# Performance work log

Hardware: AMD Instinct MI355X
Metric: run time of the kernel (lower is better)

Reference implementation:

```python
import jax, jax.numpy as jnp
import numpy as np

H, KVH, D, HID = 32, 32, 128, 4096
THETA = 10000.0
EPS = 1e-5


def setup_inputs() -> dict:
    key = jax.random.key(0)
    ks = jax.random.split(key, 7)
    T = 2048
    return {
        "positions": jnp.arange(T, dtype=jnp.int32),
        "hidden_states": jax.random.normal(ks[0], (T, HID), dtype=jnp.float32),
        "w_qkv": jax.random.normal(ks[1], ((H + 2 * KVH) * D, HID), dtype=jnp.float32) * 0.02,
        "w_o": jax.random.normal(ks[2], (HID, H * D), dtype=jnp.float32) * 0.02,
        "q_norm_w": jax.random.uniform(ks[3], (H, D), dtype=jnp.float32),
        "q_norm_b": jax.random.normal(ks[4], (H, D), dtype=jnp.float32) * 0.02,
        "k_norm_w": jax.random.uniform(ks[5], (KVH, D), dtype=jnp.float32),
        "k_norm_b": jax.random.normal(ks[6], (KVH, D), dtype=jnp.float32) * 0.02,
    }


def _per_head_ln(x, w, b):
    # x: [T, H, D]; layer_norm over last dim without affine, then *w + b (per head)
    mu = jnp.mean(x, axis=-1, keepdims=True)
    var = jnp.mean(jnp.square(x - mu), axis=-1, keepdims=True)
    xn = (x - mu) * jax.lax.rsqrt(var + EPS)
    return xn * w + b


def _rope(x, positions):
    # neox-style rotate-half RoPE; x: [T, H, D]
    half = D // 2
    inv_freq = 1.0 / (THETA ** (jnp.arange(0, D, 2, dtype=jnp.float32) / D))  # [D/2]
    freqs = positions.astype(jnp.float32)[:, None] * inv_freq  # [T, D/2]
    cos = jnp.cos(freqs)[:, None, :]  # [T, 1, D/2]
    sin = jnp.sin(freqs)[:, None, :]
    x1, x2 = x[..., :half], x[..., half:]
    return jnp.concatenate([x1 * cos - x2 * sin, x2 * cos + x1 * sin], axis=-1)


def reference(positions, hidden_states, w_qkv, w_o, q_norm_w, q_norm_b, k_norm_w, k_norm_b):
    T = hidden_states.shape[0]
    qkv = hidden_states @ w_qkv.T  # [T, (H+2*KVH)*D]
    q, k, v = jnp.split(qkv, [H * D, (H + KVH) * D], axis=-1)
    q = q.reshape(T, H, D)
    k = k.reshape(T, KVH, D)
    v = v.reshape(T, KVH, D)
    q = _per_head_ln(q, q_norm_w, q_norm_b)
    k = _per_head_ln(k, k_norm_w, k_norm_b)
    q = _rope(q, positions)
    k = _rope(k, positions)
    scale = D ** -0.5
    scores = jnp.einsum("qhd,khd->hqk", q, k) * scale  # [H, T, T]
    causal = jnp.tril(jnp.ones((T, T), dtype=bool))
    scores = jnp.where(causal, scores, jnp.finfo(scores.dtype).min)
    probs = jax.nn.softmax(scores, axis=-1)
    attn = jnp.einsum("hqk,khd->qhd", probs, v).reshape(T, H * D)
    return attn @ w_o.T  # [T, HID]
```

## Files before the change

kernel.cpp:

```cpp
#include <hip/hip_runtime.h>
#include <cstdint>

typedef unsigned short u16;
typedef __attribute__((ext_vector_type(8))) __bf16 bf16x8;
typedef __attribute__((ext_vector_type(4))) float f32x4;

__device__ __forceinline__ u16 f2bf(float f) {
  unsigned int u = __builtin_bit_cast(unsigned int, f);
  unsigned int r = (u + 0x7fffu + ((u >> 16) & 1u)) >> 16;
  return (u16)r;
}
__device__ __forceinline__ float bf2f(u16 u) {
  return __builtin_bit_cast(float, (unsigned int)u << 16);
}

__device__ __forceinline__ void gload16(const u16* g, u16* l) {
  __builtin_amdgcn_global_load_lds((const __attribute__((address_space(1))) void*)g,
                                   (__attribute__((address_space(3))) void*)l, 16, 0, 0);
}

__device__ __forceinline__ int swz64i(int row, int col) {
  return row * 64 + (((col & 0x38) ^ ((row & 7) << 3)) | (col & 7));
}
__device__ __forceinline__ int swz128i(int row, int col) {
  return row * 128 + (((col & 0x78) ^ ((row & 7) << 3)) | (col & 7));
}

__global__ __launch_bounds__(256) void cvt_bf16_kernel(const float* __restrict__ in,
                                                       u16* __restrict__ out, long n4) {
  long i = (long)blockIdx.x * 256 + threadIdx.x;
  long stride = (long)gridDim.x * 256;
  const float4* in4 = (const float4*)in;
  uint2* out2 = (uint2*)out;
  for (long k = i; k < n4; k += stride) {
    float4 v = in4[k];
    uint2 o;
    o.x = (unsigned int)f2bf(v.x) | ((unsigned int)f2bf(v.y) << 16);
    o.y = (unsigned int)f2bf(v.z) | ((unsigned int)f2bf(v.w) << 16);
    out2[k] = o;
  }
}

__global__ __launch_bounds__(512, 2) void gemm192(const u16* __restrict__ A,
                                                  const u16* __restrict__ B,
                                                  u16* __restrict__ C,
                                                  int Ndim, int Kdim) {
  extern __shared__ __align__(16) u16 lds[];
  const int tid = threadIdx.x;
  const int lane = tid & 63, wave = tid >> 6;
  const int wr = wave >> 2, wc = wave & 3;
  const int l15 = lane & 15, l4 = lane >> 4;
  const int gx = gridDim.x;
  int lin = blockIdx.y * gx + blockIdx.x;
  const int xcd = lin & 7, ii = lin >> 3;
  const int bx = xcd * (gx >> 3) + (ii >> 3), by = ii & 7;
  const long arow = (long)by * 256, brow = (long)bx * 192;
  const int NT = Kdim >> 6;

  const int rowt = tid >> 3;
  const int koff = ((tid & 7) ^ (rowt & 7)) * 8;
  const u16* gA[4];
  const u16* gB[3];
  #pragma unroll
  for (int r = 0; r < 4; ++r) gA[r] = A + (size_t)(arow + rowt + r * 64) * Kdim + koff;
  #pragma unroll
  for (int r = 0; r < 3; ++r) gB[r] = B + (size_t)(brow + rowt + r * 64) * Kdim + koff;
  u16* const ldsB = lds + 32768;

  auto STA = [&](int u) {
    u16* d = lds + (u & 1) * 16384 + tid * 8;
    #pragma unroll
    for (int r = 0; r < 4; ++r) gload16(gA[r] + (size_t)u * 64, d + r * 4096);
  };
  auto STB = [&](int u) {
    u16* d = ldsB + (u & 1) * 12288 + tid * 8;
    #pragma unroll
    for (int r = 0; r < 3; ++r) gload16(gB[r] + (size_t)u * 64, d + r * 4096);
  };

  bf16x8 af[8][2], bfr[2];
  f32x4 acc[8][3] = {};
  int cks[2];
  #pragma unroll
  for (int kc = 0; kc < 2; ++kc) cks[kc] = (((kc * 4 + l4) ^ (l15 & 7)) * 8);

  auto LDA = [&](int u) {
    const u16* base = lds + (u & 1) * 16384 + (wr * 128 + l15) * 64;
    #pragma unroll
    for (int m = 0; m < 8; ++m)
      #pragma unroll
      for (int kc = 0; kc < 2; ++kc)
        af[m][kc] = *(const bf16x8*)(base + m * 1024 + cks[kc]);
  };
  auto LDB = [&](int u, int nh) {
    const u16* base = ldsB + (u & 1) * 12288 + (wc * 48 + nh * 16 + l15) * 64;
    #pragma unroll
    for (int kc = 0; kc < 2; ++kc)
      bfr[kc] = *(const bf16x8*)(base + cks[kc]);
  };
  auto MMQ = [&](int nh) {
    #pragma unroll
    for (int kc = 0; kc < 2; ++kc)
      #pragma unroll
      for (int m = 0; m < 8; ++m)
        acc[m][nh] = __builtin_amdgcn_mfma_f32_16x16x32_bf16(af[m][kc], bfr[kc],
                                                             acc[m][nh], 0, 0, 0);
  };

#define PH_BEGIN() do { __builtin_amdgcn_s_barrier();                         \
    asm volatile("s_waitcnt lgkmcnt(0)" ::: "memory");                        \
    __builtin_amdgcn_sched_barrier(0);                                        \
    __builtin_amdgcn_s_setprio(1); } while (0)
#define PH_END() do { __builtin_amdgcn_s_setprio(0);                          \
    __builtin_amdgcn_s_barrier(); } while (0)

  STA(0); STB(0); STA(1);
  asm volatile("s_waitcnt vmcnt(4)" ::: "memory");
  __builtin_amdgcn_s_barrier();

  for (int u = 0; u < NT; ++u) {
    LDA(u); LDB(u, 0);
    if (u + 1 < NT) STB(u + 1);
    PH_BEGIN(); MMQ(0); PH_END();
    LDB(u, 1);
    if (u + 2 < NT) STA(u + 2);
    PH_BEGIN(); MMQ(1); PH_END();
    LDB(u, 2);
    PH_BEGIN(); MMQ(2);
    __builtin_amdgcn_s_setprio(0);
    if (u + 2 < NT) { asm volatile("s_waitcnt vmcnt(4)" ::: "memory"); }
    else            { asm volatile("s_waitcnt vmcnt(0)" ::: "memory"); }
    __builtin_amdgcn_s_barrier();
  }
#undef PH_BEGIN
#undef PH_END

  #pragma unroll
  for (int m = 0; m < 8; ++m)
    #pragma unroll
    for (int nh = 0; nh < 3; ++nh)
      #pragma unroll
      for (int j = 0; j < 4; ++j) {
        long r = arow + wr * 128 + m * 16 + l4 * 4 + j;
        long c = brow + wc * 48 + nh * 16 + l15;
        C[r * Ndim + c] = f2bf(acc[m][nh][j]);
      }
}

__global__ __launch_bounds__(512, 2) void gemm256(const u16* __restrict__ A,
                                                  const u16* __restrict__ B,
                                                  float* __restrict__ C,
                                                  int Ndim, int Kdim) {
  extern __shared__ __align__(16) u16 lds[];
  const int tid = threadIdx.x;
  const int lane = tid & 63, wave = tid >> 6;
  const int wr = wave >> 2, wc = wave & 3;
  const int l15 = lane & 15, l4 = lane >> 4;
  const int gx = gridDim.x;
  int lin = blockIdx.y * gx + blockIdx.x;
  const int xcd = lin & 7, ii = lin >> 3;
  const int bx = xcd * (gx >> 3) + (ii >> 3), by = ii & 7;
  const long arow = (long)by * 256, brow = (long)bx * 128;
  const int NT = Kdim >> 6;

  const int rowt = tid >> 3;
  const int koff = ((tid & 7) ^ (rowt & 7)) * 8;
  const u16* gA[4];
  const u16* gB[2];
  #pragma unroll
  for (int r = 0; r < 4; ++r) gA[r] = A + (size_t)(arow + rowt + r * 64) * Kdim + koff;
  #pragma unroll
  for (int r = 0; r < 2; ++r) gB[r] = B + (size_t)(brow + rowt + r * 64) * Kdim + koff;

  auto STA = [&](int u) {
    u16* d = lds + (u % 3) * 16384 + tid * 8;
    #pragma unroll
    for (int r = 0; r < 4; ++r) gload16(gA[r] + (size_t)u * 64, d + r * 4096);
  };
  auto STB = [&](int u) {
    u16* d = lds + 49152 + (u & 1) * 8192 + tid * 8;
    #pragma unroll
    for (int r = 0; r < 2; ++r) gload16(gB[r] + (size_t)u * 64, d + r * 4096);
  };

  bf16x8 af[4][2], bfr[2][2];
  f32x4 acc[8][2] = {};
  int cks[2];
  #pragma unroll
  for (int kc = 0; kc < 2; ++kc) cks[kc] = (((kc * 4 + l4) ^ (l15 & 7)) * 8);

  auto LDA = [&](int u, int mh) {
    const u16* base = lds + (u % 3) * 16384 + (wr * 128 + mh * 64 + l15) * 64;
    #pragma unroll
    for (int m = 0; m < 4; ++m)
      #pragma unroll
      for (int kc = 0; kc < 2; ++kc)
        af[m][kc] = *(const bf16x8*)(base + m * 1024 + cks[kc]);
  };
  auto LDB = [&](int u) {
    const u16* base = lds + 49152 + (u & 1) * 8192 + (wc * 32 + l15) * 64;
    #pragma unroll
    for (int n = 0; n < 2; ++n)
      #pragma unroll
      for (int kc = 0; kc < 2; ++kc)
        bfr[n][kc] = *(const bf16x8*)(base + n * 1024 + cks[kc]);
  };
  auto MM = [&](int mh) {
    #pragma unroll
    for (int kc = 0; kc < 2; ++kc)
      #pragma unroll
      for (int m = 0; m < 4; ++m)
        #pragma unroll
        for (int n = 0; n < 2; ++n)
          acc[mh * 4 + m][n] =
            __builtin_amdgcn_mfma_f32_16x16x32_bf16(af[m][kc], bfr[n][kc],
                                                    acc[mh * 4 + m][n], 0, 0, 0);
  };

#define PH_BEGIN() do { __builtin_amdgcn_s_barrier();                         \
    asm volatile("s_waitcnt lgkmcnt(0)" ::: "memory");                        \
    __builtin_amdgcn_sched_barrier(0);                                        \
    __builtin_amdgcn_s_setprio(1); } while (0)

  STA(0); STB(0); STA(1); STB(1);
  asm volatile("s_waitcnt vmcnt(6)" ::: "memory");
  __builtin_amdgcn_s_barrier();

  for (int u = 0; u < NT; ++u) {
    LDA(u, 0); LDB(u);
    if (u + 2 < NT) STA(u + 2);
    PH_BEGIN(); MM(0);
    __builtin_amdgcn_s_setprio(0);
    __builtin_amdgcn_s_barrier();
    LDA(u, 1);
    if (u + 2 < NT) STB(u + 2);
    PH_BEGIN(); MM(1);
    __builtin_amdgcn_s_setprio(0);
    if (u + 2 < NT) { asm volatile("s_waitcnt vmcnt(6)" ::: "memory"); }
    else if (u + 1 < NT) { asm volatile("s_waitcnt vmcnt(0)" ::: "memory"); }
    __builtin_amdgcn_s_barrier();
  }
#undef PH_BEGIN

  #pragma unroll
  for (int M = 0; M < 8; ++M)
    #pragma unroll
    for (int n = 0; n < 2; ++n)
      #pragma unroll
      for (int j = 0; j < 4; ++j) {
        long r = arow + wr * 128 + M * 16 + l4 * 4 + j;
        long c = brow + wc * 32 + n * 16 + l15;
        C[r * Ndim + c] = acc[M][n][j];
      }
}

__global__ __launch_bounds__(256) void ln_rope_kernel(
    const u16* __restrict__ qkv, const int* __restrict__ pos,
    const float* __restrict__ qw, const float* __restrict__ qb2,
    const float* __restrict__ kw, const float* __restrict__ kb2,
    u16* __restrict__ qo, u16* __restrict__ ko, u16* __restrict__ vo, int T) {
  const int hh = blockIdx.x;
  const int t = blockIdx.y * 4 + (threadIdx.x >> 6);
  const int lane = threadIdx.x & 63;
  const u16* src = qkv + (size_t)t * 12288 + hh * 128;
  u16 u1 = src[lane], u2 = src[lane + 64];
  if (hh >= 64) {
    u16* dst = vo + ((size_t)(hh - 64) * T + t) * 128;
    dst[lane] = u1; dst[lane + 64] = u2;
    return;
  }
  float x1 = bf2f(u1), x2 = bf2f(u2);
  float s = x1 + x2;
  #pragma unroll
  for (int off = 32; off; off >>= 1) s += __shfl_xor(s, off);
  float mu = s * (1.0f / 128.0f);
  float d1 = x1 - mu, d2 = x2 - mu;
  float vs = d1 * d1 + d2 * d2;
  #pragma unroll
  for (int off = 32; off; off >>= 1) vs += __shfl_xor(vs, off);
  float rstd = rsqrtf(vs * (1.0f / 128.0f) + 1e-5f);
  bool isq = hh < 32;
  int hl = isq ? hh : hh - 32;
  const float* w = (isq ? qw : kw) + hl * 128;
  const float* b = (isq ? qb2 : kb2) + hl * 128;
  float y1 = d1 * rstd * w[lane] + b[lane];
  float y2 = d2 * rstd * w[lane + 64] + b[lane + 64];
  float p = (float)pos[t];
  float invf = exp2f((float)lane * (-13.287712379549449f / 64.0f));
  float fr = p * invf;
  float sn, cs;
  __sincosf(fr, &sn, &cs);
  float o1 = y1 * cs - y2 * sn;
  float o2 = y2 * cs + y1 * sn;
  if (isq) {
    const float sc = 0.08838834764831845f;
    o1 *= sc; o2 *= sc;
    u16* dst = qo + ((size_t)hl * T + t) * 128;
    dst[lane] = f2bf(o1); dst[lane + 64] = f2bf(o2);
  } else {
    u16* dst = ko + ((size_t)hl * T + t) * 128;
    dst[lane] = f2bf(o1); dst[lane + 64] = f2bf(o2);
  }
}

__global__ __launch_bounds__(256, 2) void flash_kernel(
    const u16* __restrict__ qb, const u16* __restrict__ kb,
    const u16* __restrict__ vb, u16* __restrict__ attn, int T) {
  __shared__ __align__(16) u16 Ks[64 * 128];
  __shared__ __align__(16) u16 Vt[128 * 64];
  __shared__ __align__(16) u16 Ps[4][32 * 64];
  const int tid = threadIdx.x;
  const int lane = tid & 63, wave = tid >> 6;
  const int l15 = lane & 15, l4 = lane >> 4;
  const int h = blockIdx.y;
  const int qbase = blockIdx.x * 128;
  const u16* Q  = qb + (size_t)h * T * 128;
  const u16* Kp = kb + (size_t)h * T * 128;
  const u16* Vp = vb + (size_t)h * T * 128;
  const int rK0 = tid >> 4, d8k = (tid & 15) * 8;

  bf16x8 qf[2][4];
  #pragma unroll
  for (int mi = 0; mi < 2; ++mi)
    #pragma unroll
    for (int kc = 0; kc < 4; ++kc)
      qf[mi][kc] = *(const bf16x8*)&Q[(size_t)(qbase + mi * 64 + wave * 16 + l15) * 128 + kc * 32 + l4 * 8];

  float m_st[2][4], l_st[2][4];
  f32x4 o[2][8] = {};
  #pragma unroll
  for (int mi = 0; mi < 2; ++mi)
    #pragma unroll
    for (int j = 0; j < 4; ++j) { m_st[mi][j] = -1e30f; l_st[mi][j] = 0.0f; }

  const int ntile = (qbase + 128) / 64;
  uint4 kr[4], vr[4];
  #pragma unroll
  for (int c = 0; c < 4; ++c) {
    kr[c] = *(const uint4*)&Kp[(size_t)(rK0 + 16 * c) * 128 + d8k];
    vr[c] = *(const uint4*)&Vp[(size_t)lane * 128 + (wave + 4 * c) * 8];
  }
  for (int kt = 0; kt < ntile; ++kt) {
    const int kbase = kt * 64;
    #pragma unroll
    for (int c = 0; c < 4; ++c) {
      *(uint4*)&Ks[swz128i(rK0 + 16 * c, d8k)] = kr[c];
      const u16* pv = (const u16*)&vr[c];
      int dv = (wave + 4 * c) * 8;
      #pragma unroll
      for (int j = 0; j < 8; ++j) Vt[swz64i(dv + j, lane)] = pv[j];
    }
    __syncthreads();
    if (kt + 1 < ntile) {
      const int nb = kbase + 64;
      #pragma unroll
      for (int c = 0; c < 4; ++c) {
        kr[c] = *(const uint4*)&Kp[(size_t)(nb + rK0 + 16 * c) * 128 + d8k];
        vr[c] = *(const uint4*)&Vp[(size_t)(nb + lane) * 128 + (wave + 4 * c) * 8];
      }
    }
    #pragma unroll
    for (int mi = 0; mi < 2; ++mi) {
      const int r0 = qbase + mi * 64 + wave * 16;
      if (kbase <= r0 + 15) {
        f32x4 s[4] = {};
        __builtin_amdgcn_s_setprio(1);
        #pragma unroll
        for (int kc = 0; kc < 4; ++kc)
          #pragma unroll
          for (int nj = 0; nj < 4; ++nj) {
            bf16x8 kf = *(const bf16x8*)&Ks[swz128i(nj * 16 + l15, kc * 32 + l4 * 8)];
            s[nj] = __builtin_amdgcn_mfma_f32_16x16x32_bf16(qf[mi][kc], kf, s[nj], 0, 0, 0);
          }
        __builtin_amdgcn_s_setprio(0);
        if (kbase + 63 > r0) {
          #pragma unroll
          for (int nj = 0; nj < 4; ++nj)
            #pragma unroll
            for (int j = 0; j < 4; ++j) {
              int r = r0 + l4 * 4 + j;
              int cc = kbase + nj * 16 + l15;
              if (cc > r) s[nj][j] = -1e30f;
            }
        }
        float vmax[4];
        float dmax = -1e30f;
        #pragma unroll
        for (int j = 0; j < 4; ++j) {
          float v = fmaxf(fmaxf(s[0][j], s[1][j]), fmaxf(s[2][j], s[3][j]));
          #pragma unroll
          for (int off = 1; off < 16; off <<= 1) v = fmaxf(v, __shfl_xor(v, off));
          vmax[j] = v;
          dmax = fmaxf(dmax, v - m_st[mi][j]);
        }
        if (!__all(dmax <= 8.0f)) {
          #pragma unroll
          for (int j = 0; j < 4; ++j) {
            float mn = fmaxf(m_st[mi][j], vmax[j]);
            float scl = __expf(m_st[mi][j] - mn);
            m_st[mi][j] = mn;
            l_st[mi][j] *= scl;
            #pragma unroll
            for (int nf = 0; nf < 8; ++nf) o[mi][nf][j] *= scl;
          }
        }
        float sum[4] = {0.f, 0.f, 0.f, 0.f};
        #pragma unroll
        for (int nj = 0; nj < 4; ++nj)
          #pragma unroll
          for (int j = 0; j < 4; ++j) {
            float p = __expf(s[nj][j] - m_st[mi][j]);
            s[nj][j] = p;
            sum[j] += p;
          }
        #pragma unroll
        for (int j = 0; j < 4; ++j) {
          #pragma unroll
          for (int off = 1; off < 16; off <<= 1) sum[j] += __shfl_xor(sum[j], off);
          l_st[mi][j] += sum[j];
        }
        #pragma unroll
        for (int nj = 0; nj < 4; ++nj)
          #pragma unroll
          for (int j = 0; j < 4; ++j)
            Ps[wave][swz64i(mi * 16 + l4 * 4 + j, nj * 16 + l15)] = f2bf(s[nj][j]);
        asm volatile("s_waitcnt lgkmcnt(0)" ::: "memory");
        __builtin_amdgcn_sched_barrier(0);
        __builtin_amdgcn_s_setprio(1);
        #pragma unroll
        for (int kc = 0; kc < 2; ++kc) {
          bf16x8 pf = *(const bf16x8*)&Ps[wave][swz64i(mi * 16 + l15, kc * 32 + l4 * 8)];
          #pragma unroll
          for (int nf = 0; nf < 8; ++nf) {
            bf16x8 vf = *(const bf16x8*)&Vt[swz64i(nf * 16 + l15, kc * 32 + l4 * 8)];
            o[mi][nf] = __builtin_amdgcn_mfma_f32_16x16x32_bf16(pf, vf, o[mi][nf], 0, 0, 0);
          }
        }
        __builtin_amdgcn_s_setprio(0);
      }
    }
    __syncthreads();
  }
  #pragma unroll
  for (int mi = 0; mi < 2; ++mi) {
    float rl[4];
    #pragma unroll
    for (int j = 0; j < 4; ++j) rl[j] = 1.0f / l_st[mi][j];
    #pragma unroll
    for (int nf = 0; nf < 8; ++nf)
      #pragma unroll
      for (int j = 0; j < 4; ++j) {
        int r = qbase + mi * 64 + wave * 16 + l4 * 4 + j;
        int cc = h * 128 + nf * 16 + l15;
        attn[(size_t)r * 4096 + cc] = f2bf(o[mi][nf][j] * rl[j]);
      }
  }
}

extern "C" void kernel_launch(void* const* d_in, const int* in_sizes, int n_in,
                              void* d_out, int out_size, void* d_ws, size_t ws_size,
                              hipStream_t stream) {
  const int* positions = (const int*)d_in[0];
  const float* hidden  = (const float*)d_in[1];
  const float* w_qkv   = (const float*)d_in[2];
  const float* w_o     = (const float*)d_in[3];
  const float* qnw     = (const float*)d_in[4];
  const float* qnb     = (const float*)d_in[5];
  const float* knw     = (const float*)d_in[6];
  const float* knb     = (const float*)d_in[7];
  float* out = (float*)d_out;

  const int T = in_sizes[0];
  const int HID = 4096, NQKV = 12288, H = 32;

  char* ws = (char*)d_ws;
  u16* hid_bf  = (u16*)ws;
  u16* wreg    = (u16*)(ws + (size_t)T * HID * 2);
  u16* qkv_bf  = (u16*)(ws + (size_t)T * HID * 2 + (size_t)NQKV * HID * 2);

  u16* q_bf  = wreg;
  u16* k_bf  = q_bf + (size_t)H * T * 128;
  u16* v_bf  = k_bf + (size_t)H * T * 128;
  u16* at_bf = v_bf + (size_t)H * T * 128;
  u16* wo_bf = at_bf + (size_t)T * 4096;

  hipFuncSetAttribute(reinterpret_cast<const void*>(&gemm192),
                      hipFuncAttributeMaxDynamicSharedMemorySize, 114688);
  hipFuncSetAttribute(reinterpret_cast<const void*>(&gemm256),
                      hipFuncAttributeMaxDynamicSharedMemorySize, 131072);

  cvt_bf16_kernel<<<2048, 256, 0, stream>>>(hidden, hid_bf, (long)T * HID / 4);
  cvt_bf16_kernel<<<4096, 256, 0, stream>>>(w_qkv, wreg, (long)NQKV * HID / 4);
  gemm192<<<dim3(NQKV / 192, T / 256), 512, 114688, stream>>>(hid_bf, wreg, qkv_bf, NQKV, HID);
  ln_rope_kernel<<<dim3(96, T / 4), 256, 0, stream>>>(qkv_bf, positions, qnw, qnb, knw, knb,
                                                      q_bf, k_bf, v_bf, T);
  cvt_bf16_kernel<<<2048, 256, 0, stream>>>(w_o, wo_bf, (long)HID * HID / 4);
  flash_kernel<<<dim3(T / 128, H), 256, 0, stream>>>(q_bf, k_bf, v_bf, at_bf, T);
  gemm256<<<dim3(HID / 128, T / 256), 512, 131072, stream>>>(at_bf, wo_bf, out, HID, HID);
}
```

Measured before the change: 543.9 us.

## Triple-buffer gemm192 A tiles and pair causal q-tiles in 512-thread flash blocks

gemm192 now triple-buffers its A tile and splits each K step into two phases over 64-row halves of A instead of three phases over B column groups, so one B fragment load serves both phases. The flash kernel now runs 512 threads per block, with waves 0-3 handling a late causal q-tile and waves 4-7 an early one while sharing K/V tiles in LDS. This balances causal work across blocks and halves the K/V loads per query. The cost is more LDS per block, which may lower occupancy, and the early-tile waves sit idle on tiles beyond their causal limit.

```diff
diff --git a/kernel.cpp b/kernel.cpp
--- a/kernel.cpp
+++ b/kernel.cpp
@@ -65,10 +65,10 @@
   for (int r = 0; r < 4; ++r) gA[r] = A + (size_t)(arow + rowt + r * 64) * Kdim + koff;
   #pragma unroll
   for (int r = 0; r < 3; ++r) gB[r] = B + (size_t)(brow + rowt + r * 64) * Kdim + koff;
-  u16* const ldsB = lds + 32768;
+  u16* const ldsB = lds + 49152;
 
   auto STA = [&](int u) {
-    u16* d = lds + (u & 1) * 16384 + tid * 8;
+    u16* d = lds + (u % 3) * 16384 + tid * 8;
     #pragma unroll
     for (int r = 0; r < 4; ++r) gload16(gA[r] + (size_t)u * 64, d + r * 4096);
   };
@@ -78,33 +78,37 @@
     for (int r = 0; r < 3; ++r) gload16(gB[r] + (size_t)u * 64, d + r * 4096);
   };
 
-  bf16x8 af[8][2], bfr[2];
+  bf16x8 af[4][2], bfr[3][2];
   f32x4 acc[8][3] = {};
   int cks[2];
   #pragma unroll
   for (int kc = 0; kc < 2; ++kc) cks[kc] = (((kc * 4 + l4) ^ (l15 & 7)) * 8);
 
-  auto LDA = [&](int u) {
-    const u16* base = lds + (u & 1) * 16384 + (wr * 128 + l15) * 64;
-    #pragma unroll
-    for (int m = 0; m < 8; ++m)
+  auto LDA4 = [&](int u, int mh) {
+    const u16* base = lds + (u % 3) * 16384 + (wr * 128 + mh * 64 + l15) * 64;
+    #pragma unroll
+    for (int m = 0; m < 4; ++m)
       #pragma unroll
       for (int kc = 0; kc < 2; ++kc)
         af[m][kc] = *(const bf16x8*)(base + m * 1024 + cks[kc]);
   };
-  auto LDB = [&](int u, int nh) {
-    const u16* base = ldsB + (u & 1) * 12288 + (wc * 48 + nh * 16 + l15) * 64;
+  auto LDBall = [&](int u) {
+    const u16* base = ldsB + (u & 1) * 12288 + (wc * 48 + l15) * 64;
+    #pragma unroll
+    for (int nh = 0; nh < 3; ++nh)
+      #pragma unroll
+      for (int kc = 0; kc < 2; ++kc)
+        bfr[nh][kc] = *(const bf16x8*)(base + nh * 1024 + cks[kc]);
+  };
+  auto MM24 = [&](int mh) {
     #pragma unroll
     for (int kc = 0; kc < 2; ++kc)
-      bfr[kc] = *(const bf16x8*)(base + cks[kc]);
-  };
-  auto MMQ = [&](int nh) {
-    #pragma unroll
-    for (int kc = 0; kc < 2; ++kc)
-      #pragma unroll
-      for (int m = 0; m < 8; ++m)
-        acc[m][nh] = __builtin_amdgcn_mfma_f32_16x16x32_bf16(af[m][kc], bfr[kc],
-                                                             acc[m][nh], 0, 0, 0);
+      #pragma unroll
+      for (int m = 0; m < 4; ++m)
+        #pragma unroll
+        for (int nh = 0; nh < 3; ++nh)
+          acc[mh * 4 + m][nh] = __builtin_amdgcn_mfma_f32_16x16x32_bf16(
+              af[m][kc], bfr[nh][kc], acc[mh * 4 + m][nh], 0, 0, 0);
   };
 
 #define PH_BEGIN() do { __builtin_amdgcn_s_barrier();                         \
@@ -119,14 +123,12 @@
   __builtin_amdgcn_s_barrier();
 
   for (int u = 0; u < NT; ++u) {
-    LDA(u); LDB(u, 0);
+    LDA4(u, 0); LDBall(u);
     if (u + 1 < NT) STB(u + 1);
-    PH_BEGIN(); MMQ(0); PH_END();
-    LDB(u, 1);
+    PH_BEGIN(); MM24(0); PH_END();
+    LDA4(u, 1);
     if (u + 2 < NT) STA(u + 2);
-    PH_BEGIN(); MMQ(1); PH_END();
-    LDB(u, 2);
-    PH_BEGIN(); MMQ(2);
+    PH_BEGIN(); MM24(1);
     __builtin_amdgcn_s_setprio(0);
     if (u + 2 < NT) { asm volatile("s_waitcnt vmcnt(4)" ::: "memory"); }
     else            { asm volatile("s_waitcnt vmcnt(0)" ::: "memory"); }
@@ -303,28 +305,34 @@
   }
 }
 
-__global__ __launch_bounds__(256, 2) void flash_kernel(
+__global__ __launch_bounds__(512, 2) void flash_kernel(
     const u16* __restrict__ qb, const u16* __restrict__ kb,
     const u16* __restrict__ vb, u16* __restrict__ attn, int T) {
-  __shared__ __align__(16) u16 Ks[64 * 128];
-  __shared__ __align__(16) u16 Vt[128 * 64];
-  __shared__ __align__(16) u16 Ps[4][32 * 64];
+  extern __shared__ __align__(16) u16 flds[];
+  u16* const Ks = flds;
+  u16* const Vt = flds + 8192;
+  u16* const Ps = flds + 16384;
   const int tid = threadIdx.x;
   const int lane = tid & 63, wave = tid >> 6;
+  const int wl = wave & 3;
   const int l15 = lane & 15, l4 = lane >> 4;
   const int h = blockIdx.y;
-  const int qbase = blockIdx.x * 128;
+  const int nqt = T >> 7;
+  const int qt = (wave < 4) ? (nqt - 1 - blockIdx.x) : blockIdx.x;
+  const int qbase = qt * 128;
   const u16* Q  = qb + (size_t)h * T * 128;
   const u16* Kp = kb + (size_t)h * T * 128;
   const u16* Vp = vb + (size_t)h * T * 128;
-  const int rK0 = tid >> 4, d8k = (tid & 15) * 8;
+  const int rK = tid >> 4, d8k = (tid & 15) * 8;
+  const int rv = tid & 63, dv0 = (tid >> 6) * 8;
+  u16* const Pw = Ps + wave * 2048;
 
   bf16x8 qf[2][4];
   #pragma unroll
   for (int mi = 0; mi < 2; ++mi)
     #pragma unroll
     for (int kc = 0; kc < 4; ++kc)
-      qf[mi][kc] = *(const bf16x8*)&Q[(size_t)(qbase + mi * 64 + wave * 16 + l15) * 128 + kc * 32 + l4 * 8];
+      qf[mi][kc] = *(const bf16x8*)&Q[(size_t)(qbase + mi * 64 + wl * 16 + l15) * 128 + kc * 32 + l4 * 8];
 
   float m_st[2][4], l_st[2][4];
   f32x4 o[2][8] = {};
@@ -333,35 +341,34 @@
     #pragma unroll
     for (int j = 0; j < 4; ++j) { m_st[mi][j] = -1e30f; l_st[mi][j] = 0.0f; }
 
-  const int ntile = (qbase + 128) / 64;
-  uint4 kr[4], vr[4];
-  #pragma unroll
-  for (int c = 0; c < 4; ++c) {
-    kr[c] = *(const uint4*)&Kp[(size_t)(rK0 + 16 * c) * 128 + d8k];
-    vr[c] = *(const uint4*)&Vp[(size_t)lane * 128 + (wave + 4 * c) * 8];
+  const int ntile = 2 * (nqt - 1 - blockIdx.x) + 2;
+  uint4 kr[2], vr[2];
+  #pragma unroll
+  for (int c = 0; c < 2; ++c) {
+    kr[c] = *(const uint4*)&Kp[(size_t)(rK + 32 * c) * 128 + d8k];
+    vr[c] = *(const uint4*)&Vp[(size_t)rv * 128 + dv0 + 64 * c];
   }
   for (int kt = 0; kt < ntile; ++kt) {
     const int kbase = kt * 64;
     #pragma unroll
-    for (int c = 0; c < 4; ++c) {
-      *(uint4*)&Ks[swz128i(rK0 + 16 * c, d8k)] = kr[c];
+    for (int c = 0; c < 2; ++c) {
+      *(uint4*)&Ks[swz128i(rK + 32 * c, d8k)] = kr[c];
       const u16* pv = (const u16*)&vr[c];
-      int dv = (wave + 4 * c) * 8;
-      #pragma unroll
-      for (int j = 0; j < 8; ++j) Vt[swz64i(dv + j, lane)] = pv[j];
+      #pragma unroll
+      for (int j = 0; j < 8; ++j) Vt[swz64i(dv0 + 64 * c + j, rv)] = pv[j];
     }
     __syncthreads();
     if (kt + 1 < ntile) {
       const int nb = kbase + 64;
       #pragma unroll
-      for (int c = 0; c < 4; ++c) {
-        kr[c] = *(const uint4*)&Kp[(size_t)(nb + rK0 + 16 * c) * 128 + d8k];
-        vr[c] = *(const uint4*)&Vp[(size_t)(nb + lane) * 128 + (wave + 4 * c) * 8];
+      for (int c = 0; c < 2; ++c) {
+        kr[c] = *(const uint4*)&Kp[(size_t)(nb + rK + 32 * c) * 128 + d8k];
+        vr[c] = *(const uint4*)&Vp[(size_t)(nb + rv) * 128 + dv0 + 64 * c];
       }
     }
     #pragma unroll
     for (int mi = 0; mi < 2; ++mi) {
-      const int r0 = qbase + mi * 64 + wave * 16;
+      const int r0 = qbase + mi * 64 + wl * 16;
       if (kbase <= r0 + 15) {
         f32x4 s[4] = {};
         __builtin_amdgcn_s_setprio(1);
@@ -423,13 +430,13 @@
         for (int nj = 0; nj < 4; ++nj)
           #pragma unroll
           for (int j = 0; j < 4; ++j)
-            Ps[wave][swz64i(mi * 16 + l4 * 4 + j, nj * 16 + l15)] = f2bf(s[nj][j]);
+            Pw[swz64i(mi * 16 + l4 * 4 + j, nj * 16 + l15)] = f2bf(s[nj][j]);
         asm volatile("s_waitcnt lgkmcnt(0)" ::: "memory");
         __builtin_amdgcn_sched_barrier(0);
         __builtin_amdgcn_s_setprio(1);
         #pragma unroll
         for (int kc = 0; kc < 2; ++kc) {
-          bf16x8 pf = *(const bf16x8*)&Ps[wave][swz64i(mi * 16 + l15, kc * 32 + l4 * 8)];
+          bf16x8 pf = *(const bf16x8*)&Pw[swz64i(mi * 16 + l15, kc * 32 + l4 * 8)];
           #pragma unroll
           for (int nf = 0; nf < 8; ++nf) {
             bf16x8 vf = *(const bf16x8*)&Vt[swz64i(nf * 16 + l15, kc * 32 + l4 * 8)];
@@ -450,7 +457,7 @@
     for (int nf = 0; nf < 8; ++nf)
       #pragma unroll
       for (int j = 0; j < 4; ++j) {
-        int r = qbase + mi * 64 + wave * 16 + l4 * 4 + j;
+        int r = qbase + mi * 64 + wl * 16 + l4 * 4 + j;
         int cc = h * 128 + nf * 16 + l15;
         attn[(size_t)r * 4096 + cc] = f2bf(o[mi][nf][j] * rl[j]);
       }
@@ -485,16 +492,18 @@
   u16* wo_bf = at_bf + (size_t)T * 4096;
 
   hipFuncSetAttribute(reinterpret_cast<const void*>(&gemm192),
-                      hipFuncAttributeMaxDynamicSharedMemorySize, 114688);
+                      hipFuncAttributeMaxDynamicSharedMemorySize, 147456);
   hipFuncSetAttribute(reinterpret_cast<const void*>(&gemm256),
                       hipFuncAttributeMaxDynamicSharedMemorySize, 131072);
+  hipFuncSetAttribute(reinterpret_cast<const void*>(&flash_kernel),
+                      hipFuncAttributeMaxDynamicSharedMemorySize, 65536);
 
   cvt_bf16_kernel<<<2048, 256, 0, stream>>>(hidden, hid_bf, (long)T * HID / 4);
   cvt_bf16_kernel<<<4096, 256, 0, stream>>>(w_qkv, wreg, (long)NQKV * HID / 4);
-  gemm192<<<dim3(NQKV / 192, T / 256), 512, 114688, stream>>>(hid_bf, wreg, qkv_bf, NQKV, HID);
+  gemm192<<<dim3(NQKV / 192, T / 256), 512, 147456, stream>>>(hid_bf, wreg, qkv_bf, NQKV, HID);
   ln_rope_kernel<<<dim3(96, T / 4), 256, 0, stream>>>(qkv_bf, positions, qnw, qnb, knw, knb,
                                                       q_bf, k_bf, v_bf, T);
   cvt_bf16_kernel<<<2048, 256, 0, stream>>>(w_o, wo_bf, (long)HID * HID / 4);
-  flash_kernel<<<dim3(T / 128, H), 256, 0, stream>>>(q_bf, k_bf, v_bf, at_bf, T);
+  flash_kernel<<<dim3(T / 256, H), 512, 65536, stream>>>(q_bf, k_bf, v_bf, at_bf, T);
   gemm256<<<dim3(HID / 128, T / 256), 512, 131072, stream>>>(at_bf, wo_bf, out, HID, HID);
 }
```

Result: faster. 498.6 us (-8.3%).
